# Kernel tuning notes

Measured on AMD Instinct MI355X. Metric: run time of the kernel, lower is better.

## Reference

```python
import jax, jax.numpy as jnp
import numpy as np

DIM = 2048
H = 16          # n_heads
HKV = 4         # n_kv_heads
NREP = H // HKV
ROPE_D = 64
NOPE_D = 128
V_D = 128
QK_D = ROPE_D + NOPE_D
KV_RANK = 512
Q_RANK = 1536
B, T = 2, 2048


def _rope_cache(seq_len, head_dim, dtype=jnp.float32):
    # theta over even dims, angles concatenated [ang, ang] -> [T, head_dim]
    theta = 1.0 / (10000.0 ** (jnp.arange(0, head_dim, 2, dtype=dtype) / head_dim))
    pos = jnp.arange(seq_len, dtype=dtype)
    ang = jnp.outer(pos, theta)
    ang = jnp.concatenate([ang, ang], axis=-1)
    return jnp.cos(ang), jnp.sin(ang)  # each [T, head_dim]


def _rotate_half(x):
    half = x.shape[-1] // 2
    return jnp.concatenate([-x[..., half:], x[..., :half]], axis=-1)


def _apply_rope(x, cos, sin):
    # x: [B, T, h, d]; cos/sin: [T, d] broadcast over batch and heads
    return x * cos[None, :, None, :] + _rotate_half(x) * sin[None, :, None, :]


def setup_inputs() -> dict:
    key = jax.random.key(0)
    ks = jax.random.split(key, 9)
    s = 0.02
    return {
        "x": jax.random.normal(ks[0], (B, T, DIM), jnp.float32),
        "W_kv_down": jax.random.normal(ks[1], (DIM, KV_RANK), jnp.float32) * s,
        "W_k_nope": jax.random.normal(ks[2], (KV_RANK, HKV * NOPE_D), jnp.float32) * s,
        "W_k_rope": jax.random.normal(ks[3], (KV_RANK, HKV * ROPE_D), jnp.float32) * s,
        "W_v": jax.random.normal(ks[4], (KV_RANK, HKV * V_D), jnp.float32) * s,
        "W_q_down": jax.random.normal(ks[5], (DIM, Q_RANK), jnp.float32) * s,
        "W_q_nope": jax.random.normal(ks[6], (Q_RANK, H * NOPE_D), jnp.float32) * s,
        "W_q_rope": jax.random.normal(ks[7], (Q_RANK, H * ROPE_D), jnp.float32) * s,
        "W_o": jax.random.normal(ks[8], (H * V_D, DIM), jnp.float32) * s,
    }


def reference(x, W_kv_down, W_k_nope, W_k_rope, W_v, W_q_down, W_q_nope, W_q_rope, W_o):
    Bx, Tx, _ = x.shape
    scale = 1.0 / np.sqrt(QK_D)

    kv_c = x @ W_kv_down                                        # [B,T,KV_RANK]
    k_nope = (kv_c @ W_k_nope).reshape(Bx, Tx, HKV, NOPE_D)
    k_rope = (kv_c @ W_k_rope).reshape(Bx, Tx, HKV, ROPE_D)
    v = (kv_c @ W_v).reshape(Bx, Tx, HKV, V_D)

    q_c = x @ W_q_down                                          # [B,T,Q_RANK]
    q_nope = (q_c @ W_q_nope).reshape(Bx, Tx, H, NOPE_D)
    q_rope = (q_c @ W_q_rope).reshape(Bx, Tx, H, ROPE_D)

    cos, sin = _rope_cache(Tx, ROPE_D, x.dtype)
    q_rope = _apply_rope(q_rope, cos, sin)
    k_rope = _apply_rope(k_rope, cos, sin)

    q = jnp.concatenate([q_nope, q_rope], axis=-1).transpose(0, 2, 1, 3)  # [B,H,T,QK_D]
    k = jnp.concatenate([k_nope, k_rope], axis=-1).transpose(0, 2, 1, 3)  # [B,HKV,T,QK_D]
    vh = v.transpose(0, 2, 1, 3)                                          # [B,HKV,T,V_D]

    k = jnp.repeat(k, NREP, axis=1)   # GQA repeat -> [B,H,T,QK_D]
    vh = jnp.repeat(vh, NREP, axis=1)

    attn = jnp.einsum("bhqd,bhkd->bhqk", q, k) * scale
    causal = jnp.triu(jnp.ones((Tx, Tx), dtype=bool), k=1)
    attn = jnp.where(causal[None, None], -jnp.inf, attn)
    attn = jax.nn.softmax(attn, axis=-1)

    out = jnp.einsum("bhqk,bhkd->bhqd", attn, vh)               # [B,H,T,V_D]
    out = out.transpose(0, 2, 1, 3).reshape(Bx, Tx, H * V_D)
    return out @ W_o
```

## Files before the change

### kernel.cpp

```cpp
#include <hip/hip_runtime.h>
#include <hip/hip_bf16.h>

typedef __bf16 bf16;
typedef __attribute__((ext_vector_type(8))) __bf16 bf16x8;
typedef __attribute__((ext_vector_type(4))) __bf16 bf16x4;
typedef __attribute__((ext_vector_type(2))) __bf16 bf16x2;
typedef __attribute__((ext_vector_type(4))) float f32x4;

#define NH 16
#define NKV 4
#define ROPE_DIM 64
#define NOPE_DIM 128
#define V_DIM 128
#define QK_DIM 192
#define TT 2048
#define BB 2
#define MM 4096

#define QK_SCALE 0.07216878364870323f

__device__ __forceinline__ void gload16(const bf16* g, bf16* l) {
    __builtin_amdgcn_global_load_lds(
        (const __attribute__((address_space(1))) void*)g,
        (__attribute__((address_space(3))) void*)l, 16, 0, 0);
}

struct PrepArgs {
    const float* wsrc[8];
    bf16* wdst[8];
    const float* x;
    bf16* xb;
    float* ct;
    float* st;
};

__global__ __launch_bounds__(256) void k_prep(PrepArgs a) {
    constexpr int WR[8] = {2048, 2048, 512, 512, 512, 1536, 1536, 2048};
    constexpr int WC[8] = {512, 1536, 512, 256, 512, 2048, 1024, 2048};
    const int bid = blockIdx.x;
    if (bid < 13440) {
        int w = 0, base = 0;
        #pragma unroll
        for (int i = 0; i < 8; i++) {
            int t = (WC[i] >> 5) * (WR[i] >> 5);
            if (w == i && bid >= base + t) { base += t; w = i + 1; }
        }
        const int local = bid - base;
        const int R = WR[w], C = WC[w];
        const int tilesX = C >> 5;
        const int tyt = local / tilesX, txt = local - tyt * tilesX;
        const int c0 = txt * 32, r0 = tyt * 32;
        const float* s = a.wsrc[w];
        bf16* d = a.wdst[w];
        __shared__ float tile[32][33];
        int tx = threadIdx.x & 31, ty = threadIdx.x >> 5;
        #pragma unroll
        for (int rr = ty; rr < 32; rr += 8)
            tile[rr][tx] = s[(size_t)(r0 + rr) * C + c0 + tx];
        __syncthreads();
        #pragma unroll
        for (int q = threadIdx.x; q < 512; q += 256) {
            int ccq = q >> 4, pr = (q & 15) << 1;
            bf16x2 v;
            v[0] = (bf16)tile[pr][ccq];
            v[1] = (bf16)tile[pr + 1][ccq];
            *(bf16x2*)&d[(size_t)(c0 + ccq) * R + r0 + pr] = v;
        }
    } else if (bid < 13696) {
        int idx = (bid - 13440) * 256 + threadIdx.x;
        int t = idx >> 5, i = idx & 31;
        float theta = powf(10000.f, -(float)(2 * i) / 64.f);
        float ang = (float)t * theta;
        a.ct[idx] = cosf(ang);
        a.st[idx] = sinf(ang);
    } else {
        int i = (bid - 13696) * 256 + threadIdx.x;
        float4 v = *(const float4*)(a.x + (size_t)i * 4);
        bf16* o = a.xb + (size_t)i * 4;
        o[0] = (bf16)v.x; o[1] = (bf16)v.y; o[2] = (bf16)v.z; o[3] = (bf16)v.w;
    }
}

template<int EPI>
__global__ __launch_bounds__(256) void k_gemm(const bf16* __restrict__ A, int lda,
                                              const bf16* __restrict__ Bt, int ldb,
                                              void* __restrict__ Cv, int ldc, int K,
                                              const float* __restrict__ ct,
                                              const float* __restrict__ st,
                                              bf16* __restrict__ vt) {
    __shared__ __align__(16) bf16 As[2][128 * 32];
    __shared__ __align__(16) bf16 Bs[2][128 * 32];
    const int tid = threadIdx.x;
    const int lane = tid & 63;
    const int wid = tid >> 6;
    const int wr = wid >> 1, wc = wid & 1;
    const int g = lane >> 4, c = lane & 15;
    const int m0 = blockIdx.y * 128, n0 = blockIdx.x * 128;

    f32x4 acc[4][4] = {};
    const int rdswz = (g ^ ((c >> 1) & 3)) * 8;

    auto stage = [&](int buf, int k0) {
        #pragma unroll
        for (int i = 0; i < 2; i++) {
            int ch = tid + 256 * i;
            int row = ch >> 2;
            int kc = (ch & 3) ^ ((ch >> 3) & 3);
            gload16(A + (size_t)(m0 + row) * lda + k0 + kc * 8, &As[buf][ch * 8]);
            gload16(Bt + (size_t)(n0 + row) * ldb + k0 + kc * 8, &Bs[buf][ch * 8]);
        }
    };

    stage(0, 0);
    __syncthreads();
    const int nt = K >> 5;
    for (int t = 0; t < nt; ++t) {
        const int cur = t & 1;
        if (t + 1 < nt) stage(cur ^ 1, (t + 1) << 5);
        bf16x8 af[4], bfr[4];
        #pragma unroll
        for (int i = 0; i < 4; i++)
            af[i] = *(const bf16x8*)&As[cur][(wr * 64 + i * 16 + c) * 32 + rdswz];
        #pragma unroll
        for (int j = 0; j < 4; j++)
            bfr[j] = *(const bf16x8*)&Bs[cur][(wc * 64 + j * 16 + c) * 32 + rdswz];
        #pragma unroll
        for (int i = 0; i < 4; i++)
            #pragma unroll
            for (int j = 0; j < 4; j++)
                acc[i][j] = __builtin_amdgcn_mfma_f32_16x16x32_bf16(
                    af[i], bfr[j], acc[i][j], 0, 0, 0);
        __syncthreads();
    }

    if constexpr (EPI <= 1) {
        #pragma unroll
        for (int i = 0; i < 4; i++) {
            int row = m0 + wr * 64 + i * 16 + g * 4;
            #pragma unroll
            for (int j = 0; j < 4; j++) {
                int col = n0 + wc * 64 + j * 16 + c;
                #pragma unroll
                for (int r = 0; r < 4; r++) {
                    if (EPI == 1)
                        ((float*)Cv)[(size_t)(row + r) * ldc + col] = acc[i][j][r];
                    else
                        ((bf16*)Cv)[(size_t)(row + r) * ldc + col] = (bf16)acc[i][j][r];
                }
            }
        }
    } else if constexpr (EPI == 2) {
        bf16* ka = (bf16*)Cv;
        #pragma unroll
        for (int i = 0; i < 4; i++) {
            int row = m0 + wr * 64 + i * 16 + g * 4;
            int bq = row >> 11, t0 = row & 2047;
            #pragma unroll
            for (int j = 0; j < 4; j++) {
                int col = n0 + wc * 64 + j * 16 + c;
                if (col < 512) {
                    int h = col >> 7, d = col & 127;
                    bf16* dst = ka + ((size_t)(bq * NKV + h) * TT + t0) * QK_DIM + d;
                    #pragma unroll
                    for (int r = 0; r < 4; r++) dst[r * QK_DIM] = (bf16)acc[i][j][r];
                } else if (col < 768) {
                    int cr = col - 512;
                    int h = cr >> 6, dr = cr & 63, ia = dr & 31;
                    float sgn = (dr < 32) ? -1.f : 1.f;
                    bf16* dst = ka + ((size_t)(bq * NKV + h) * TT + t0) * QK_DIM + 128 + dr;
                    #pragma unroll
                    for (int r = 0; r < 4; r++) {
                        float cs = ct[(t0 + r) * 32 + ia], sn = st[(t0 + r) * 32 + ia];
                        dst[r * QK_DIM] = (bf16)(acc[i][j][r] * cs + sgn * acc[i][j ^ 2][r] * sn);
                    }
                } else {
                    int cr = col - 768;
                    int h = cr >> 7, d = cr & 127;
                    bf16x4 pk;
                    #pragma unroll
                    for (int r = 0; r < 4; r++) pk[r] = (bf16)acc[i][j][r];
                    *(bf16x4*)&vt[((size_t)((bq * NKV + h) * V_DIM + d)) * TT + t0] = pk;
                }
            }
        }
    } else {
        bf16* qa = (bf16*)Cv;
        #pragma unroll
        for (int i = 0; i < 4; i++) {
            int row = m0 + wr * 64 + i * 16 + g * 4;
            int bq = row >> 11, t0 = row & 2047;
            #pragma unroll
            for (int j = 0; j < 4; j++) {
                int col = n0 + wc * 64 + j * 16 + c;
                if (col < 2048) {
                    int h = col >> 7, d = col & 127;
                    bf16* dst = qa + ((size_t)(bq * NH + h) * TT + t0) * QK_DIM + d;
                    #pragma unroll
                    for (int r = 0; r < 4; r++)
                        dst[r * QK_DIM] = (bf16)(acc[i][j][r] * QK_SCALE);
                } else {
                    int cr = col - 2048;
                    int h = cr >> 6, dr = cr & 63, ia = dr & 31;
                    float sgn = (dr < 32) ? -1.f : 1.f;
                    bf16* dst = qa + ((size_t)(bq * NH + h) * TT + t0) * QK_DIM + 128 + dr;
                    #pragma unroll
                    for (int r = 0; r < 4; r++) {
                        float cs = ct[(t0 + r) * 32 + ia], sn = st[(t0 + r) * 32 + ia];
                        dst[r * QK_DIM] =
                            (bf16)((acc[i][j][r] * cs + sgn * acc[i][j ^ 2][r] * sn) * QK_SCALE);
                    }
                }
            }
        }
    }
}

__global__ __launch_bounds__(256, 2) void k_attn(const bf16* __restrict__ qa,
                                                 const bf16* __restrict__ ka,
                                                 const bf16* __restrict__ vt,
                                                 bf16* __restrict__ out) {
    __shared__ __align__(16) bf16 Klds[64 * QK_DIM];
    __shared__ __align__(16) bf16 Vlds[128 * 64];
    __shared__ __align__(16) bf16 Plds[4][32 * 64];

    const int tid  = threadIdx.x;
    const int lane = tid & 63;
    const int wid  = tid >> 6;
    const int g = lane >> 4, c = lane & 15;
    const int hsw = c & 7;

    const int qi = (blockIdx.y & 16) ? (15 - (int)blockIdx.x) : (int)blockIdx.x;
    const int q0 = qi * 128;
    const int bh = blockIdx.y;
    const int b = bh >> 4, h = bh & 15;
    const int kv = b * NKV + (h >> 2);
    const int qb0 = q0 + wid * 32;

    bf16x8 qf[2][6];
    #pragma unroll
    for (int qs = 0; qs < 2; ++qs) {
        const bf16* qp = qa + ((size_t)bh * TT + qb0 + qs * 16 + c) * QK_DIM + g * 8;
        #pragma unroll
        for (int cc = 0; cc < 6; ++cc) qf[qs][cc] = *(const bf16x8*)(qp + cc * 32);
    }

    f32x4 accO[2][8] = {};
    float l[2] = {0.f, 0.f};

    const bf16* kbase = ka + (size_t)kv * TT * QK_DIM;
    const bf16* vbase = vt + (size_t)kv * V_DIM * TT;

    const int nk = 2 * qi + 2;
    for (int it = 0; it < nk; ++it) {
        const int k0 = it * 64;
        __syncthreads();
        #pragma unroll
        for (int i = 0; i < 6; ++i) {
            int ch = tid + 256 * i;
            int row = ch / 24, cs = ch % 24;
            int gc = cs ^ (row & 7);
            gload16(kbase + (size_t)(k0 + row) * QK_DIM + gc * 8, &Klds[ch * 8]);
        }
        #pragma unroll
        for (int i = 0; i < 4; ++i) {
            int ch = tid + 256 * i;
            int row = ch >> 3, cs = ch & 7;
            int gc = cs ^ (row & 7);
            gload16(vbase + (size_t)row * TT + k0 + gc * 8, &Vlds[ch * 8]);
        }
        __syncthreads();

        if (k0 > qb0 + 15) continue;
        const bool a1 = (k0 <= qb0 + 31);

        f32x4 s[2][4] = {};
        #pragma unroll
        for (int cc = 0; cc < 6; ++cc) {
            #pragma unroll
            for (int j = 0; j < 4; ++j) {
                bf16x8 kf = *(const bf16x8*)&Klds[(j * 16 + c) * QK_DIM +
                                                  ((4 * cc + g) ^ hsw) * 8];
                s[0][j] = __builtin_amdgcn_mfma_f32_16x16x32_bf16(kf, qf[0][cc], s[0][j], 0, 0, 0);
                s[1][j] = __builtin_amdgcn_mfma_f32_16x16x32_bf16(kf, qf[1][cc], s[1][j], 0, 0, 0);
            }
        }

        #pragma unroll
        for (int qs = 0; qs < 2; ++qs) {
            if (qs == 1 && !a1) break;
            const int qb = qb0 + qs * 16;
            if (k0 + 63 > qb) {
                #pragma unroll
                for (int j = 0; j < 4; ++j)
                    #pragma unroll
                    for (int r = 0; r < 4; ++r)
                        if (k0 + j * 16 + g * 4 + r > qb + c) s[qs][j][r] = -1e30f;
            }
            float ps = 0.f;
            #pragma unroll
            for (int j = 0; j < 4; ++j) {
                bf16x4 pk;
                #pragma unroll
                for (int r = 0; r < 4; ++r) {
                    float e = __expf(s[qs][j][r]);
                    ps += e;
                    pk[r] = (bf16)e;
                }
                *(bf16x4*)&Plds[wid][(qs * 16 + c) * 64 +
                                     ((j * 16 + g * 4) ^ (hsw * 8))] = pk;
            }
            ps += __shfl_xor(ps, 16, 64);
            ps += __shfl_xor(ps, 32, 64);
            l[qs] += ps;
        }

        if (a1) {
            #pragma unroll
            for (int kc = 0; kc < 2; ++kc) {
                bf16x8 pf0 = *(const bf16x8*)&Plds[wid][(c)      * 64 + ((kc * 32 + g * 8) ^ (hsw * 8))];
                bf16x8 pf1 = *(const bf16x8*)&Plds[wid][(16 + c) * 64 + ((kc * 32 + g * 8) ^ (hsw * 8))];
                #pragma unroll
                for (int nj = 0; nj < 8; ++nj) {
                    bf16x8 vf = *(const bf16x8*)&Vlds[(nj * 16 + c) * 64 +
                                                      ((4 * kc + g) ^ hsw) * 8];
                    accO[0][nj] = __builtin_amdgcn_mfma_f32_16x16x32_bf16(vf, pf0, accO[0][nj], 0, 0, 0);
                    accO[1][nj] = __builtin_amdgcn_mfma_f32_16x16x32_bf16(vf, pf1, accO[1][nj], 0, 0, 0);
                }
            }
        } else {
            #pragma unroll
            for (int kc = 0; kc < 2; ++kc) {
                bf16x8 pf0 = *(const bf16x8*)&Plds[wid][(c) * 64 + ((kc * 32 + g * 8) ^ (hsw * 8))];
                #pragma unroll
                for (int nj = 0; nj < 8; ++nj) {
                    bf16x8 vf = *(const bf16x8*)&Vlds[(nj * 16 + c) * 64 +
                                                      ((4 * kc + g) ^ hsw) * 8];
                    accO[0][nj] = __builtin_amdgcn_mfma_f32_16x16x32_bf16(vf, pf0, accO[0][nj], 0, 0, 0);
                }
            }
        }
    }

    #pragma unroll
    for (int qs = 0; qs < 2; ++qs) {
        float inv = 1.f / l[qs];
        size_t rowoff = ((size_t)(b * TT + qb0 + qs * 16 + c)) * (NH * V_DIM) + h * V_DIM;
        #pragma unroll
        for (int nj = 0; nj < 8; ++nj) {
            bf16x4 o;
            #pragma unroll
            for (int r = 0; r < 4; ++r) o[r] = (bf16)(accO[qs][nj][r] * inv);
            *(bf16x4*)&out[rowoff + nj * 16 + g * 4] = o;
        }
    }
}

extern "C" void kernel_launch(void* const* d_in, const int* in_sizes, int n_in,
                              void* d_out, int out_size, void* d_ws, size_t ws_size,
                              hipStream_t stream) {
    const float* x    = (const float*)d_in[0];

    char* p = (char*)d_ws;
    size_t off = 0;
    auto take = [&](size_t elems, size_t esz) -> void* {
        void* r = p + off;
        off += ((elems * esz + 255) / 256) * 256;
        return r;
    };

    bf16* XB  = (bf16*)take((size_t)MM * 2048, 2);
    bf16* BT1 = (bf16*)take((size_t)2048 * 2048, 2);
    bf16* BT2 = (bf16*)take((size_t)1280 * 512, 2);
    bf16* BT3 = (bf16*)take((size_t)3072 * 1536, 2);
    bf16* BTO = (bf16*)take((size_t)2048 * 2048, 2);
    bf16* C1  = (bf16*)take((size_t)MM * 2048, 2);
    bf16* QA  = (bf16*)take((size_t)BB * NH * TT * QK_DIM, 2);
    bf16* KA  = (bf16*)take((size_t)BB * NKV * TT * QK_DIM, 2);
    bf16* VT  = (bf16*)take((size_t)BB * NKV * V_DIM * TT, 2);
    bf16* AO  = (bf16*)take((size_t)MM * 2048, 2);
    float* CT = (float*)take((size_t)TT * 32, 4);
    float* ST = (float*)take((size_t)TT * 32, 4);
    (void)ws_size; (void)in_sizes; (void)n_in; (void)out_size;

    PrepArgs pa;
    pa.wsrc[0] = (const float*)d_in[1]; pa.wdst[0] = BT1;
    pa.wsrc[1] = (const float*)d_in[5]; pa.wdst[1] = BT1 + (size_t)512 * 2048;
    pa.wsrc[2] = (const float*)d_in[2]; pa.wdst[2] = BT2;
    pa.wsrc[3] = (const float*)d_in[3]; pa.wdst[3] = BT2 + (size_t)512 * 512;
    pa.wsrc[4] = (const float*)d_in[4]; pa.wdst[4] = BT2 + (size_t)768 * 512;
    pa.wsrc[5] = (const float*)d_in[6]; pa.wdst[5] = BT3;
    pa.wsrc[6] = (const float*)d_in[7]; pa.wdst[6] = BT3 + (size_t)2048 * 1536;
    pa.wsrc[7] = (const float*)d_in[8]; pa.wdst[7] = BTO;
    pa.x = x; pa.xb = XB; pa.ct = CT; pa.st = ST;
    k_prep<<<21888, 256, 0, stream>>>(pa);

    k_gemm<0><<<dim3(16, 32), 256, 0, stream>>>(XB, 2048, BT1, 2048, C1, 2048, 2048,
                                                nullptr, nullptr, nullptr);
    k_gemm<2><<<dim3(10, 32), 256, 0, stream>>>(C1, 2048, BT2, 512, KA, 0, 512,
                                                CT, ST, VT);
    k_gemm<3><<<dim3(24, 32), 256, 0, stream>>>(C1 + 512, 2048, BT3, 1536, QA, 0, 1536,
                                                CT, ST, nullptr);

    k_attn<<<dim3(16, BB * NH), 256, 0, stream>>>(QA, KA, VT, AO);

    k_gemm<1><<<dim3(16, 32), 256, 0, stream>>>(AO, 2048, BTO, 2048, d_out, 2048, 2048,
                                                nullptr, nullptr, nullptr);
}
```

Baseline: 381.3 us.

## Merge K/V and Q up-projection GEMMs and keep attention P in registers

Combines the two up-projection GEMM launches into a single 1088-block kernel via a shared device-side gemm_body, which fills the GPU better and removes one launch. In attention, K rows are loaded in permuted order so that the QK^T accumulator layout matches the B-operand layout of the PV MFMA. That lets the softmax probabilities be packed directly in registers instead of going through a per-wave LDS buffer, cutting LDS traffic and shared memory use. Launch bounds for attention are raised to 3 blocks per SM to exploit the freed LDS, with the risk of register pressure or spills.

```diff
diff --git a/kernel.cpp b/kernel.cpp
--- a/kernel.cpp
+++ b/kernel.cpp
@@ -82,6 +82,139 @@
 }
 
 template<int EPI>
+__device__ __forceinline__ void gemm_body(
+        bf16 (*As)[128 * 32], bf16 (*Bs)[128 * 32], int bx, int by,
+        const bf16* __restrict__ A, int lda,
+        const bf16* __restrict__ Bt, int ldb,
+        void* __restrict__ Cv, int ldc, int K,
+        const float* __restrict__ ct, const float* __restrict__ st,
+        bf16* __restrict__ vt) {
+    const int tid = threadIdx.x;
+    const int lane = tid & 63;
+    const int wid = tid >> 6;
+    const int wr = wid >> 1, wc = wid & 1;
+    const int g = lane >> 4, c = lane & 15;
+    const int m0 = by * 128, n0 = bx * 128;
+
+    f32x4 acc[4][4] = {};
+    const int rdswz = (g ^ ((c >> 1) & 3)) * 8;
+
+    auto stage = [&](int buf, int k0) {
+        #pragma unroll
+        for (int i = 0; i < 2; i++) {
+            int ch = tid + 256 * i;
+            int row = ch >> 2;
+            int kc = (ch & 3) ^ ((ch >> 3) & 3);
+            gload16(A + (size_t)(m0 + row) * lda + k0 + kc * 8, &As[buf][ch * 8]);
+            gload16(Bt + (size_t)(n0 + row) * ldb + k0 + kc * 8, &Bs[buf][ch * 8]);
+        }
+    };
+
+    stage(0, 0);
+    __syncthreads();
+    const int nt = K >> 5;
+    for (int t = 0; t < nt; ++t) {
+        const int cur = t & 1;
+        if (t + 1 < nt) stage(cur ^ 1, (t + 1) << 5);
+        bf16x8 af[4], bfr[4];
+        #pragma unroll
+        for (int i = 0; i < 4; i++)
+            af[i] = *(const bf16x8*)&As[cur][(wr * 64 + i * 16 + c) * 32 + rdswz];
+        #pragma unroll
+        for (int j = 0; j < 4; j++)
+            bfr[j] = *(const bf16x8*)&Bs[cur][(wc * 64 + j * 16 + c) * 32 + rdswz];
+        #pragma unroll
+        for (int i = 0; i < 4; i++)
+            #pragma unroll
+            for (int j = 0; j < 4; j++)
+                acc[i][j] = __builtin_amdgcn_mfma_f32_16x16x32_bf16(
+                    af[i], bfr[j], acc[i][j], 0, 0, 0);
+        __syncthreads();
+    }
+
+    if constexpr (EPI <= 1) {
+        #pragma unroll
+        for (int i = 0; i < 4; i++) {
+            int row = m0 + wr * 64 + i * 16 + g * 4;
+            #pragma unroll
+            for (int j = 0; j < 4; j++) {
+                int col = n0 + wc * 64 + j * 16 + c;
+                #pragma unroll
+                for (int r = 0; r < 4; r++) {
+                    if (EPI == 1)
+                        ((float*)Cv)[(size_t)(row + r) * ldc + col] = acc[i][j][r];
+                    else
+                        ((bf16*)Cv)[(size_t)(row + r) * ldc + col] = (bf16)acc[i][j][r];
+                }
+            }
+        }
+    } else if constexpr (EPI == 2) {
+        bf16* ka = (bf16*)Cv;
+        #pragma unroll
+        for (int i = 0; i < 4; i++) {
+            int row = m0 + wr * 64 + i * 16 + g * 4;
+            int bq = row >> 11, t0 = row & 2047;
+            #pragma unroll
+            for (int j = 0; j < 4; j++) {
+                int col = n0 + wc * 64 + j * 16 + c;
+                if (col < 512) {
+                    int h = col >> 7, d = col & 127;
+                    bf16* dst = ka + ((size_t)(bq * NKV + h) * TT + t0) * QK_DIM + d;
+                    #pragma unroll
+                    for (int r = 0; r < 4; r++) dst[r * QK_DIM] = (bf16)acc[i][j][r];
+                } else if (col < 768) {
+                    int cr = col - 512;
+                    int h = cr >> 6, dr = cr & 63, ia = dr & 31;
+                    float sgn = (dr < 32) ? -1.f : 1.f;
+                    bf16* dst = ka + ((size_t)(bq * NKV + h) * TT + t0) * QK_DIM + 128 + dr;
+                    #pragma unroll
+                    for (int r = 0; r < 4; r++) {
+                        float cs = ct[(t0 + r) * 32 + ia], sn = st[(t0 + r) * 32 + ia];
+                        dst[r * QK_DIM] = (bf16)(acc[i][j][r] * cs + sgn * acc[i][j ^ 2][r] * sn);
+                    }
+                } else {
+                    int cr = col - 768;
+                    int h = cr >> 7, d = cr & 127;
+                    bf16x4 pk;
+                    #pragma unroll
+                    for (int r = 0; r < 4; r++) pk[r] = (bf16)acc[i][j][r];
+                    *(bf16x4*)&vt[((size_t)((bq * NKV + h) * V_DIM + d)) * TT + t0] = pk;
+                }
+            }
+        }
+    } else {
+        bf16* qa = (bf16*)Cv;
+        #pragma unroll
+        for (int i = 0; i < 4; i++) {
+            int row = m0 + wr * 64 + i * 16 + g * 4;
+            int bq = row >> 11, t0 = row & 2047;
+            #pragma unroll
+            for (int j = 0; j < 4; j++) {
+                int col = n0 + wc * 64 + j * 16 + c;
+                if (col < 2048) {
+                    int h = col >> 7, d = col & 127;
+                    bf16* dst = qa + ((size_t)(bq * NH + h) * TT + t0) * QK_DIM + d;
+                    #pragma unroll
+                    for (int r = 0; r < 4; r++)
+                        dst[r * QK_DIM] = (bf16)(acc[i][j][r] * QK_SCALE);
+                } else {
+                    int cr = col - 2048;
+                    int h = cr >> 6, dr = cr & 63, ia = dr & 31;
+                    float sgn = (dr < 32) ? -1.f : 1.f;
+                    bf16* dst = qa + ((size_t)(bq * NH + h) * TT + t0) * QK_DIM + 128 + dr;
+                    #pragma unroll
+                    for (int r = 0; r < 4; r++) {
+                        float cs = ct[(t0 + r) * 32 + ia], sn = st[(t0 + r) * 32 + ia];
+                        dst[r * QK_DIM] =
+                            (bf16)((acc[i][j][r] * cs + sgn * acc[i][j ^ 2][r] * sn) * QK_SCALE);
+                    }
+                }
+            }
+        }
+    }
+}
+
+template<int EPI>
 __global__ __launch_bounds__(256) void k_gemm(const bf16* __restrict__ A, int lda,
                                               const bf16* __restrict__ Bt, int ldb,
                                               void* __restrict__ Cv, int ldc, int K,
@@ -90,138 +223,35 @@
                                               bf16* __restrict__ vt) {
     __shared__ __align__(16) bf16 As[2][128 * 32];
     __shared__ __align__(16) bf16 Bs[2][128 * 32];
-    const int tid = threadIdx.x;
-    const int lane = tid & 63;
-    const int wid = tid >> 6;
-    const int wr = wid >> 1, wc = wid & 1;
-    const int g = lane >> 4, c = lane & 15;
-    const int m0 = blockIdx.y * 128, n0 = blockIdx.x * 128;
-
-    f32x4 acc[4][4] = {};
-    const int rdswz = (g ^ ((c >> 1) & 3)) * 8;
-
-    auto stage = [&](int buf, int k0) {
-        #pragma unroll
-        for (int i = 0; i < 2; i++) {
-            int ch = tid + 256 * i;
-            int row = ch >> 2;
-            int kc = (ch & 3) ^ ((ch >> 3) & 3);
-            gload16(A + (size_t)(m0 + row) * lda + k0 + kc * 8, &As[buf][ch * 8]);
-            gload16(Bt + (size_t)(n0 + row) * ldb + k0 + kc * 8, &Bs[buf][ch * 8]);
-        }
-    };
-
-    stage(0, 0);
-    __syncthreads();
-    const int nt = K >> 5;
-    for (int t = 0; t < nt; ++t) {
-        const int cur = t & 1;
-        if (t + 1 < nt) stage(cur ^ 1, (t + 1) << 5);
-        bf16x8 af[4], bfr[4];
-        #pragma unroll
-        for (int i = 0; i < 4; i++)
-            af[i] = *(const bf16x8*)&As[cur][(wr * 64 + i * 16 + c) * 32 + rdswz];
-        #pragma unroll
-        for (int j = 0; j < 4; j++)
-            bfr[j] = *(const bf16x8*)&Bs[cur][(wc * 64 + j * 16 + c) * 32 + rdswz];
-        #pragma unroll
-        for (int i = 0; i < 4; i++)
-            #pragma unroll
-            for (int j = 0; j < 4; j++)
-                acc[i][j] = __builtin_amdgcn_mfma_f32_16x16x32_bf16(
-                    af[i], bfr[j], acc[i][j], 0, 0, 0);
-        __syncthreads();
-    }
-
-    if constexpr (EPI <= 1) {
-        #pragma unroll
-        for (int i = 0; i < 4; i++) {
-            int row = m0 + wr * 64 + i * 16 + g * 4;
-            #pragma unroll
-            for (int j = 0; j < 4; j++) {
-                int col = n0 + wc * 64 + j * 16 + c;
-                #pragma unroll
-                for (int r = 0; r < 4; r++) {
-                    if (EPI == 1)
-                        ((float*)Cv)[(size_t)(row + r) * ldc + col] = acc[i][j][r];
-                    else
-                        ((bf16*)Cv)[(size_t)(row + r) * ldc + col] = (bf16)acc[i][j][r];
-                }
-            }
-        }
-    } else if constexpr (EPI == 2) {
-        bf16* ka = (bf16*)Cv;
-        #pragma unroll
-        for (int i = 0; i < 4; i++) {
-            int row = m0 + wr * 64 + i * 16 + g * 4;
-            int bq = row >> 11, t0 = row & 2047;
-            #pragma unroll
-            for (int j = 0; j < 4; j++) {
-                int col = n0 + wc * 64 + j * 16 + c;
-                if (col < 512) {
-                    int h = col >> 7, d = col & 127;
-                    bf16* dst = ka + ((size_t)(bq * NKV + h) * TT + t0) * QK_DIM + d;
-                    #pragma unroll
-                    for (int r = 0; r < 4; r++) dst[r * QK_DIM] = (bf16)acc[i][j][r];
-                } else if (col < 768) {
-                    int cr = col - 512;
-                    int h = cr >> 6, dr = cr & 63, ia = dr & 31;
-                    float sgn = (dr < 32) ? -1.f : 1.f;
-                    bf16* dst = ka + ((size_t)(bq * NKV + h) * TT + t0) * QK_DIM + 128 + dr;
-                    #pragma unroll
-                    for (int r = 0; r < 4; r++) {
-                        float cs = ct[(t0 + r) * 32 + ia], sn = st[(t0 + r) * 32 + ia];
-                        dst[r * QK_DIM] = (bf16)(acc[i][j][r] * cs + sgn * acc[i][j ^ 2][r] * sn);
-                    }
-                } else {
-                    int cr = col - 768;
-                    int h = cr >> 7, d = cr & 127;
-                    bf16x4 pk;
-                    #pragma unroll
-                    for (int r = 0; r < 4; r++) pk[r] = (bf16)acc[i][j][r];
-                    *(bf16x4*)&vt[((size_t)((bq * NKV + h) * V_DIM + d)) * TT + t0] = pk;
-                }
-            }
-        }
+    gemm_body<EPI>(As, Bs, blockIdx.x, blockIdx.y, A, lda, Bt, ldb, Cv, ldc, K, ct, st, vt);
+}
+
+__global__ __launch_bounds__(256) void k_gemm23(const bf16* __restrict__ C1,
+                                                const bf16* __restrict__ BT2,
+                                                const bf16* __restrict__ BT3,
+                                                bf16* __restrict__ KA,
+                                                bf16* __restrict__ QA,
+                                                bf16* __restrict__ VT,
+                                                const float* __restrict__ ct,
+                                                const float* __restrict__ st) {
+    __shared__ __align__(16) bf16 As[2][128 * 32];
+    __shared__ __align__(16) bf16 Bs[2][128 * 32];
+    const int bid = blockIdx.x;
+    if (bid < 320) {
+        gemm_body<2>(As, Bs, bid % 10, bid / 10, C1, 2048, BT2, 512, KA, 0, 512, ct, st, VT);
     } else {
-        bf16* qa = (bf16*)Cv;
-        #pragma unroll
-        for (int i = 0; i < 4; i++) {
-            int row = m0 + wr * 64 + i * 16 + g * 4;
-            int bq = row >> 11, t0 = row & 2047;
-            #pragma unroll
-            for (int j = 0; j < 4; j++) {
-                int col = n0 + wc * 64 + j * 16 + c;
-                if (col < 2048) {
-                    int h = col >> 7, d = col & 127;
-                    bf16* dst = qa + ((size_t)(bq * NH + h) * TT + t0) * QK_DIM + d;
-                    #pragma unroll
-                    for (int r = 0; r < 4; r++)
-                        dst[r * QK_DIM] = (bf16)(acc[i][j][r] * QK_SCALE);
-                } else {
-                    int cr = col - 2048;
-                    int h = cr >> 6, dr = cr & 63, ia = dr & 31;
-                    float sgn = (dr < 32) ? -1.f : 1.f;
-                    bf16* dst = qa + ((size_t)(bq * NH + h) * TT + t0) * QK_DIM + 128 + dr;
-                    #pragma unroll
-                    for (int r = 0; r < 4; r++) {
-                        float cs = ct[(t0 + r) * 32 + ia], sn = st[(t0 + r) * 32 + ia];
-                        dst[r * QK_DIM] =
-                            (bf16)((acc[i][j][r] * cs + sgn * acc[i][j ^ 2][r] * sn) * QK_SCALE);
-                    }
-                }
-            }
-        }
-    }
-}
-
-__global__ __launch_bounds__(256, 2) void k_attn(const bf16* __restrict__ qa,
+        const int b2 = bid - 320;
+        gemm_body<3>(As, Bs, b2 % 24, b2 / 24, C1 + 512, 2048, BT3, 1536, QA, 0, 1536,
+                     ct, st, nullptr);
+    }
+}
+
+__global__ __launch_bounds__(256, 3) void k_attn(const bf16* __restrict__ qa,
                                                  const bf16* __restrict__ ka,
                                                  const bf16* __restrict__ vt,
                                                  bf16* __restrict__ out) {
     __shared__ __align__(16) bf16 Klds[64 * QK_DIM];
     __shared__ __align__(16) bf16 Vlds[128 * 64];
-    __shared__ __align__(16) bf16 Plds[4][32 * 64];
 
     const int tid  = threadIdx.x;
     const int lane = tid & 63;
@@ -250,6 +280,9 @@
     const bf16* kbase = ka + (size_t)kv * TT * QK_DIM;
     const bf16* vbase = vt + (size_t)kv * V_DIM * TT;
 
+    union PW { bf16x2 h; unsigned u; };
+    union PF { bf16x8 v; unsigned u[4]; };
+
     const int nk = 2 * qi + 2;
     for (int it = 0; it < nk; ++it) {
         const int k0 = it * 64;
@@ -259,7 +292,9 @@
             int ch = tid + 256 * i;
             int row = ch / 24, cs = ch % 24;
             int gc = cs ^ (row & 7);
-            gload16(kbase + (size_t)(k0 + row) * QK_DIM + gc * 8, &Klds[ch * 8]);
+            int jl = row >> 4, gl = (row >> 2) & 3, rl = row & 3;
+            int psrc = 32 * (jl >> 1) + 8 * gl + 4 * (jl & 1) + rl;
+            gload16(kbase + (size_t)(k0 + psrc) * QK_DIM + gc * 8, &Klds[ch * 8]);
         }
         #pragma unroll
         for (int i = 0; i < 4; ++i) {
@@ -285,57 +320,60 @@
             }
         }
 
+        PW pw[2][4][2];
         #pragma unroll
         for (int qs = 0; qs < 2; ++qs) {
             if (qs == 1 && !a1) break;
             const int qb = qb0 + qs * 16;
             if (k0 + 63 > qb) {
                 #pragma unroll
-                for (int j = 0; j < 4; ++j)
+                for (int j = 0; j < 4; ++j) {
+                    const int kbase2 = k0 + 32 * (j >> 1) + 4 * (j & 1) + 8 * g;
                     #pragma unroll
                     for (int r = 0; r < 4; ++r)
-                        if (k0 + j * 16 + g * 4 + r > qb + c) s[qs][j][r] = -1e30f;
+                        if (kbase2 + r > qb + c) s[qs][j][r] = -1e30f;
+                }
             }
             float ps = 0.f;
             #pragma unroll
             for (int j = 0; j < 4; ++j) {
-                bf16x4 pk;
-                #pragma unroll
-                for (int r = 0; r < 4; ++r) {
-                    float e = __expf(s[qs][j][r]);
-                    ps += e;
-                    pk[r] = (bf16)e;
-                }
-                *(bf16x4*)&Plds[wid][(qs * 16 + c) * 64 +
-                                     ((j * 16 + g * 4) ^ (hsw * 8))] = pk;
+                float e0 = __expf(s[qs][j][0]);
+                float e1 = __expf(s[qs][j][1]);
+                float e2 = __expf(s[qs][j][2]);
+                float e3 = __expf(s[qs][j][3]);
+                ps += (e0 + e1) + (e2 + e3);
+                PW a, bb;
+                a.h[0] = (bf16)e0; a.h[1] = (bf16)e1;
+                bb.h[0] = (bf16)e2; bb.h[1] = (bf16)e3;
+                pw[qs][j][0] = a;
+                pw[qs][j][1] = bb;
             }
             ps += __shfl_xor(ps, 16, 64);
             ps += __shfl_xor(ps, 32, 64);
             l[qs] += ps;
         }
 
-        if (a1) {
-            #pragma unroll
-            for (int kc = 0; kc < 2; ++kc) {
-                bf16x8 pf0 = *(const bf16x8*)&Plds[wid][(c)      * 64 + ((kc * 32 + g * 8) ^ (hsw * 8))];
-                bf16x8 pf1 = *(const bf16x8*)&Plds[wid][(16 + c) * 64 + ((kc * 32 + g * 8) ^ (hsw * 8))];
+        #pragma unroll
+        for (int kc = 0; kc < 2; ++kc) {
+            PF pf0, pf1;
+            pf0.u[0] = pw[0][2 * kc][0].u;     pf0.u[1] = pw[0][2 * kc][1].u;
+            pf0.u[2] = pw[0][2 * kc + 1][0].u; pf0.u[3] = pw[0][2 * kc + 1][1].u;
+            pf1.u[0] = pw[1][2 * kc][0].u;     pf1.u[1] = pw[1][2 * kc][1].u;
+            pf1.u[2] = pw[1][2 * kc + 1][0].u; pf1.u[3] = pw[1][2 * kc + 1][1].u;
+            if (a1) {
                 #pragma unroll
                 for (int nj = 0; nj < 8; ++nj) {
                     bf16x8 vf = *(const bf16x8*)&Vlds[(nj * 16 + c) * 64 +
                                                       ((4 * kc + g) ^ hsw) * 8];
-                    accO[0][nj] = __builtin_amdgcn_mfma_f32_16x16x32_bf16(vf, pf0, accO[0][nj], 0, 0, 0);
-                    accO[1][nj] = __builtin_amdgcn_mfma_f32_16x16x32_bf16(vf, pf1, accO[1][nj], 0, 0, 0);
-                }
-            }
-        } else {
-            #pragma unroll
-            for (int kc = 0; kc < 2; ++kc) {
-                bf16x8 pf0 = *(const bf16x8*)&Plds[wid][(c) * 64 + ((kc * 32 + g * 8) ^ (hsw * 8))];
+                    accO[0][nj] = __builtin_amdgcn_mfma_f32_16x16x32_bf16(vf, pf0.v, accO[0][nj], 0, 0, 0);
+                    accO[1][nj] = __builtin_amdgcn_mfma_f32_16x16x32_bf16(vf, pf1.v, accO[1][nj], 0, 0, 0);
+                }
+            } else {
                 #pragma unroll
                 for (int nj = 0; nj < 8; ++nj) {
                     bf16x8 vf = *(const bf16x8*)&Vlds[(nj * 16 + c) * 64 +
                                                       ((4 * kc + g) ^ hsw) * 8];
-                    accO[0][nj] = __builtin_amdgcn_mfma_f32_16x16x32_bf16(vf, pf0, accO[0][nj], 0, 0, 0);
+                    accO[0][nj] = __builtin_amdgcn_mfma_f32_16x16x32_bf16(vf, pf0.v, accO[0][nj], 0, 0, 0);
                 }
             }
         }
@@ -396,10 +434,7 @@
 
     k_gemm<0><<<dim3(16, 32), 256, 0, stream>>>(XB, 2048, BT1, 2048, C1, 2048, 2048,
                                                 nullptr, nullptr, nullptr);
-    k_gemm<2><<<dim3(10, 32), 256, 0, stream>>>(C1, 2048, BT2, 512, KA, 0, 512,
-                                                CT, ST, VT);
-    k_gemm<3><<<dim3(24, 32), 256, 0, stream>>>(C1 + 512, 2048, BT3, 1536, QA, 0, 1536,
-                                                CT, ST, nullptr);
+    k_gemm23<<<1088, 256, 0, stream>>>(C1, BT2, BT3, KA, QA, VT, CT, ST);
 
     k_attn<<<dim3(16, BB * NH), 256, 0, stream>>>(QA, KA, VT, AO);
 
```

Result: slower. 520.1 us (+36.4%).
